# Performance work log

Measured on AMD Instinct MI355X. Metric: run time of the kernel, lower is better.

Reference implementation:

```python
import jax, jax.numpy as jnp
import numpy as np

B, N, C, H = 8, 2048, 512, 8
D = C // H                      # head dim = 64
Q_LENGTHS = [1024 + 128 * i for i in range(B)]  # ragged: 1024..1920, sum below
TQ = sum(Q_LENGTHS)             # 11776 total queries


def setup_inputs() -> dict:
    key = jax.random.key(0)
    ks = jax.random.split(key, 5)
    w = 0.02  # init scale for weights
    return {
        "x": jax.random.normal(ks[0], (B, N, C), jnp.float32),
        "q": jax.random.normal(ks[1], (TQ, C), jnp.float32),
        "Wq": jax.random.normal(ks[2], (C, C), jnp.float32) * w,
        "Wkv": jax.random.normal(ks[3], (2 * C, C), jnp.float32) * w,
        "Wproj": jax.random.normal(ks[4], (C, C), jnp.float32) * w,
        "bproj": jnp.zeros((C,), jnp.float32),
        "q_lengths": jnp.array(Q_LENGTHS, jnp.int32),
        "max_q_len": max(Q_LENGTHS),
    }


def reference(x, q, Wq, Wkv, Wproj, bproj, q_lengths, max_q_len):
    # Eval path of Attention.forward: batched_sparse_attention(q, k, v, q_lengths, scale)
    # == varlen cross-attention: queries of batch b attend over all N kv tokens of batch b.
    Tq = q.shape[0]
    scale = D ** -0.5

    qh = (q @ Wq.T).reshape(Tq, H, D)                 # [Tq, H, D]
    kv = (x @ Wkv.T).reshape(B, N, 2, H, D)
    k = kv[:, :, 0]                                   # [B, N, H, D]
    v = kv[:, :, 1]                                   # [B, N, H, D]

    # ragged -> padded per-batch layout
    csum = jnp.cumsum(q_lengths)                      # [B]
    offs = jnp.concatenate([jnp.zeros((1,), csum.dtype), csum])
    tok = jnp.arange(Tq)
    q_batch = (tok[:, None] >= csum[None, :]).sum(-1)  # [Tq] batch id per query
    q_pos = tok - offs[q_batch]                        # [Tq] position within batch

    qpad = jnp.zeros((B, max_q_len, H, D), qh.dtype).at[q_batch, q_pos].set(qh)

    scores = jnp.einsum('blhd,bnhd->bhln', qpad, k) * scale  # [B, H, L, N]
    attn = jax.nn.softmax(scores, axis=-1)                   # all N keys valid
    out = jnp.einsum('bhln,bnhd->blhd', attn, v)             # [B, L, H, D]

    out = out[q_batch, q_pos].reshape(Tq, C)           # gather ragged rows back
    return out @ Wproj.T + bproj
```

## Files before the change

### kernel.cpp

```cpp
#include <hip/hip_runtime.h>
#include <hip/hip_bf16.h>
#include <math.h>

constexpr int Cc = 512;
constexpr int Hh = 8;
constexpr int Dd = 64;
constexpr int Nn = 2048;
constexpr int Bb = 8;
constexpr int GK = 512;

typedef __attribute__((ext_vector_type(8))) short short8;
typedef __attribute__((ext_vector_type(4))) float f32x4;
typedef __attribute__((ext_vector_type(4))) unsigned int u32x4;
typedef __attribute__((ext_vector_type(2))) unsigned int u32x2;

#define C2SCALE 0.1803368801f

static __device__ __forceinline__ ushort f2bf(float v) {
  __hip_bfloat16 h = __float2bfloat16(v);
  return *reinterpret_cast<ushort*>(&h);
}
static __device__ __forceinline__ float bf2f(ushort u) {
  __hip_bfloat16 h = *reinterpret_cast<__hip_bfloat16*>(&u);
  return __bfloat162float(h);
}
static __device__ __forceinline__ unsigned int pk2(float f0, float f1) {
  return (unsigned int)f2bf(f0) | ((unsigned int)f2bf(f1) << 16);
}

template <int MODE, int TERMS, bool AF32, bool BF32>
__global__ __launch_bounds__(256) void mfma_nt2_kernel(
    const void* __restrict__ A0p, const void* __restrict__ A1p,
    const void* __restrict__ B0p, const void* __restrict__ B1p,
    const float* __restrict__ bias, float* __restrict__ Cf,
    ushort* __restrict__ Chi, int Nc)
{
  __shared__ ushort lAh[128 * 32];
  __shared__ ushort lBh[128 * 32];
  __shared__ ushort lAl[TERMS == 3 ? 128 * 32 : 1];
  __shared__ ushort lBl[TERMS == 3 ? 128 * 32 : 1];

  const int tid = threadIdx.x;
  const int w = tid >> 6, lane = tid & 63;
  const int c = lane & 15, g = lane >> 4;
  const int wr = (w >> 1) * 64, wc = (w & 1) * 64;
  const int m0 = blockIdx.y * 128, n0 = blockIdx.x * 128;
  const int sr = tid >> 2;
  const int sk = (tid & 3) * 8;

  short8 rAh[2], rAl[2], rBh[2], rBl[2];

  auto ldf32 = [&](const float* F, size_t idx, short8& h, short8& l) {
    const float4 f0 = *(const float4*)(F + idx);
    const float4 f1 = *(const float4*)(F + idx + 4);
    const float vv[8] = {f0.x, f0.y, f0.z, f0.w, f1.x, f1.y, f1.z, f1.w};
#pragma unroll
    for (int j = 0; j < 8; ++j) {
      const ushort hb = f2bf(vv[j]);
      ((ushort*)&h)[j] = hb;
      if (TERMS == 3) ((ushort*)&l)[j] = f2bf(vv[j] - bf2f(hb));
    }
  };

  auto loadA = [&](int k0) {
#pragma unroll
    for (int hf = 0; hf < 2; ++hf) {
      const size_t idx = (size_t)(m0 + sr + hf * 64) * GK + k0 + sk;
      if (AF32) {
        ldf32((const float*)A0p, idx, rAh[hf], rAl[hf]);
      } else {
        rAh[hf] = *(const short8*)((const ushort*)A0p + idx);
        if (TERMS == 3) rAl[hf] = *(const short8*)((const ushort*)A1p + idx);
      }
    }
  };
  auto loadB = [&](int k0) {
#pragma unroll
    for (int hf = 0; hf < 2; ++hf) {
      const size_t idx = (size_t)(n0 + sr + hf * 64) * GK + k0 + sk;
      if (BF32) {
        ldf32((const float*)B0p, idx, rBh[hf], rBl[hf]);
      } else {
        rBh[hf] = *(const short8*)((const ushort*)B0p + idx);
        if (TERMS == 3) rBl[hf] = *(const short8*)((const ushort*)B1p + idx);
      }
    }
  };

  f32x4 acc[4][4] = {};
  loadA(0);
  loadB(0);

  for (int k0 = 0; k0 < GK; k0 += 32) {
    __syncthreads();
    *(short8*)&lAh[sr * 32 + sk]        = rAh[0];
    *(short8*)&lAh[(sr + 64) * 32 + sk] = rAh[1];
    *(short8*)&lBh[sr * 32 + sk]        = rBh[0];
    *(short8*)&lBh[(sr + 64) * 32 + sk] = rBh[1];
    if (TERMS == 3) {
      *(short8*)&lAl[sr * 32 + sk]        = rAl[0];
      *(short8*)&lAl[(sr + 64) * 32 + sk] = rAl[1];
      *(short8*)&lBl[sr * 32 + sk]        = rBl[0];
      *(short8*)&lBl[(sr + 64) * 32 + sk] = rBl[1];
    }
    __syncthreads();
    if (k0 + 32 < GK) { loadA(k0 + 32); loadB(k0 + 32); }

    short8 ah[4], al[4], bh[4], bl[4];
#pragma unroll
    for (int i = 0; i < 4; ++i) {
      const int ar = (wr + i * 16 + c) * 32 + g * 8;
      const int br = (wc + i * 16 + c) * 32 + g * 8;
      ah[i] = *(const short8*)&lAh[ar];
      bh[i] = *(const short8*)&lBh[br];
      if (TERMS == 3) {
        al[i] = *(const short8*)&lAl[ar];
        bl[i] = *(const short8*)&lBl[br];
      }
    }
#pragma unroll
    for (int mi = 0; mi < 4; ++mi)
#pragma unroll
      for (int nj = 0; nj < 4; ++nj) {
        if (TERMS == 3) {
          acc[mi][nj] = __builtin_amdgcn_mfma_f32_16x16x32_bf16(ah[mi], bl[nj], acc[mi][nj], 0,0,0);
          acc[mi][nj] = __builtin_amdgcn_mfma_f32_16x16x32_bf16(al[mi], bh[nj], acc[mi][nj], 0,0,0);
        }
        acc[mi][nj] = __builtin_amdgcn_mfma_f32_16x16x32_bf16(ah[mi], bh[nj], acc[mi][nj], 0,0,0);
      }
  }

#pragma unroll
  for (int mi = 0; mi < 4; ++mi) {
#pragma unroll
    for (int r = 0; r < 4; ++r) {
      const size_t rb = (size_t)(m0 + wr + mi * 16 + g * 4 + r) * Nc;
#pragma unroll
      for (int nj = 0; nj < 4; ++nj) {
        const int col = n0 + wc + nj * 16 + c;
        const float v = acc[mi][nj][r];
        if (MODE == 0) {
          Cf[rb + col] = v + bias[col];
        } else if (MODE == 1) {
          Chi[rb + col] = f2bf(v);
        } else {
          Chi[rb + col] = f2bf(v * C2SCALE);
        }
      }
    }
  }
}

__global__ __launch_bounds__(512, 4) void attn_mfma11_kernel(
    const ushort* __restrict__ qhi,
    const ushort* __restrict__ kbf,
    const ushort* __restrict__ vtb,
    ushort* __restrict__ ohi,
    ushort* __restrict__ olo)
{
  constexpr int QOFF[8] = {0, 1024, 2176, 3456, 4864, 6400, 8064, 9856};

  const int lin = blockIdx.x;
  const int b  = lin & 7;
  const int h  = (lin >> 3) & 7;
  const int qt = lin >> 6;

  const int Lb  = 1024 + 128 * b;
  const int off = QOFF[b];
  if (qt * 128 >= Lb) return;

  constexpr int KP = 72;
  constexpr int VP = 136;
  constexpr int NC = Nn / 128;
  __shared__ ushort Ks[128 * KP];
  __shared__ ushort Vs[64 * VP];

  const int tid = threadIdx.x;
  const int lane = tid & 63;
  const int w = tid >> 6;
  const int c = lane & 15;
  const int g = (lane >> 4) & 3;

  short8 qf[2];
  const int qrow = off + qt * 128 + w * 16 + c;
  {
    const size_t base = (size_t)qrow * Cc + h * Dd + g * 8;
    qf[0] = *(const short8*)(qhi + base);
    qf[1] = *(const short8*)(qhi + base + 32);
  }

  float l_part = 0.f;
  f32x4 accO4[4] = {};

  const size_t kbase = (size_t)b * Nn * Cc + h * Dd;
  const size_t vbase = (size_t)h * Dd * (Bb * Nn) + (size_t)b * Nn;

  for (int ch = 0; ch < NC; ++ch) {
    __syncthreads();
#pragma unroll
    for (int it = 0; it < 2; ++it) {
      const int i = tid + it * 512;
      const int row = i >> 3, c8 = (i & 7) * 8;
      *(short8*)&Ks[row * KP + c8] =
          *(const short8*)&kbf[kbase + (size_t)(ch * 128 + row) * Cc + c8];
    }
#pragma unroll
    for (int it = 0; it < 2; ++it) {
      const int i = tid + it * 512;
      const int row = i >> 4, c8 = (i & 15) * 8;
      const int kb1 = (c8 & ~31) | (((c8 >> 3) & 3) << 2);
      const size_t gb = vbase + (size_t)row * (Bb * Nn) + ch * 128;
      const u32x2 vlo = *(const u32x2*)&vtb[gb + kb1];
      const u32x2 vhi = *(const u32x2*)&vtb[gb + kb1 + 16];
      u32x4 vv;
      vv[0] = vlo[0]; vv[1] = vlo[1];
      vv[2] = vhi[0]; vv[3] = vhi[1];
      *(short8*)&Vs[row * VP + c8] = __builtin_bit_cast(short8, vv);
    }
    __syncthreads();

#pragma unroll
    for (int st = 0; st < 2; ++st) {
      f32x4 accT4[4] = {};
      __builtin_amdgcn_s_setprio(1);
#pragma unroll
      for (int ks2 = 0; ks2 < 2; ++ks2) {
#pragma unroll
        for (int kb = 0; kb < 4; ++kb) {
          const short8 kf = *(const short8*)
              &Ks[(st * 64 + kb * 16 + c) * KP + ks2 * 32 + g * 8];
          accT4[kb] = __builtin_amdgcn_mfma_f32_16x16x32_bf16(kf, qf[ks2], accT4[kb], 0,0,0);
        }
      }
      __builtin_amdgcn_s_setprio(0);

      unsigned int up[4][2];
#pragma unroll
      for (int kb = 0; kb < 4; ++kb) {
        const float p0 = __builtin_amdgcn_exp2f(accT4[kb][0]);
        const float p1 = __builtin_amdgcn_exp2f(accT4[kb][1]);
        const float p2 = __builtin_amdgcn_exp2f(accT4[kb][2]);
        const float p3 = __builtin_amdgcn_exp2f(accT4[kb][3]);
        l_part += (p0 + p1) + (p2 + p3);
        up[kb][0] = pk2(p0, p1);
        up[kb][1] = pk2(p2, p3);
      }

#pragma unroll
      for (int ks2 = 0; ks2 < 2; ++ks2) {
        u32x4 wv;
        wv.x = up[2 * ks2][0];
        wv.y = up[2 * ks2][1];
        wv.z = up[2 * ks2 + 1][0];
        wv.w = up[2 * ks2 + 1][1];
        const short8 pa = __builtin_bit_cast(short8, wv);
        __builtin_amdgcn_s_setprio(1);
#pragma unroll
        for (int db = 0; db < 4; ++db) {
          const short8 vf = *(const short8*)
              &Vs[(db * 16 + c) * VP + st * 64 + ks2 * 32 + g * 8];
          accO4[db] = __builtin_amdgcn_mfma_f32_16x16x32_bf16(vf, pa, accO4[db], 0,0,0);
        }
        __builtin_amdgcn_s_setprio(0);
      }
    }
  }

  float l = l_part;
  l += __shfl_xor(l, 16);
  l += __shfl_xor(l, 32);
  const float inv = 1.f / l;
  const size_t rb = (size_t)qrow * Cc + h * Dd;
#pragma unroll
  for (int db = 0; db < 4; ++db) {
    const int d0 = db * 16 + g * 4;
    ushort4 uh, ul;
#pragma unroll
    for (int e = 0; e < 4; ++e) {
      const float o = accO4[db][e] * inv;
      const ushort hb = f2bf(o);
      ((ushort*)&uh)[e] = hb;
      ((ushort*)&ul)[e] = f2bf(o - bf2f(hb));
    }
    *(ushort4*)&ohi[rb + d0] = uh;
    *(ushort4*)&olo[rb + d0] = ul;
  }
}

extern "C" void kernel_launch(void* const* d_in, const int* in_sizes, int n_in,
                              void* d_out, int out_size, void* d_ws, size_t ws_size,
                              hipStream_t stream)
{
  const float* x     = (const float*)d_in[0];
  const float* q     = (const float*)d_in[1];
  const float* Wq    = (const float*)d_in[2];
  const float* Wkv   = (const float*)d_in[3];
  const float* Wproj = (const float*)d_in[4];
  const float* bproj = (const float*)d_in[5];

  const int TQ = in_sizes[1] / Cc;
  const int BN = in_sizes[0] / Cc;

  const float* Wv = Wkv + (size_t)Cc * Cc;

  const size_t szQ = (size_t)TQ * Cc * 2;
  const size_t szX = (size_t)BN * Cc * 2;

  char* p = (char*)d_ws;
  ushort* q_hi  = (ushort*)p;  p += szQ;
  ushort* k_bf  = (ushort*)p;  p += szX;
  ushort* v_t   = (ushort*)p;  p += szX;
  ushort* at_hi = (ushort*)p;  p += szQ;
  ushort* at_lo = (ushort*)p;

  mfma_nt2_kernel<2, 1, true, true><<<dim3(Cc/128, TQ/128), 256, 0, stream>>>(
      q, nullptr, Wq, nullptr, nullptr, nullptr, q_hi, Cc);
  mfma_nt2_kernel<1, 1, true, true><<<dim3(Cc/128, BN/128), 256, 0, stream>>>(
      x, nullptr, Wkv, nullptr, nullptr, nullptr, k_bf, Cc);
  mfma_nt2_kernel<1, 1, true, true><<<dim3(BN/128, Cc/128), 256, 0, stream>>>(
      Wv, nullptr, x, nullptr, nullptr, nullptr, v_t, BN);
  attn_mfma11_kernel<<<dim3(64 * 15), 512, 0, stream>>>(
      q_hi, k_bf, v_t, at_hi, at_lo);
  mfma_nt2_kernel<0, 3, false, true><<<dim3(Cc/128, TQ/128), 256, 0, stream>>>(
      at_hi, at_lo, Wproj, nullptr, bproj, (float*)d_out, nullptr, Cc);
}
```

Measured before the change: 191.5 us.

## Have each attention wave handle two 16-query tiles, halving block threads

The attention kernel now runs 256 threads per block instead of 512. Each wave processes 32 query rows as two 16-row tiles and reuses every K and V fragment read from LDS for two MFMAs. This halves LDS fragment reads per MFMA and the per-row share of synchronisation. In exchange it doubles the accumulator and probability registers per thread, which may hurt occupancy, and each thread issues twice as many global loads to fill the K/V tiles.

```diff
diff --git a/kernel.cpp b/kernel.cpp
--- a/kernel.cpp
+++ b/kernel.cpp
@@ -151,7 +151,7 @@
   }
 }
 
-__global__ __launch_bounds__(512, 4) void attn_mfma11_kernel(
+__global__ __launch_bounds__(256, 4) void attn_mfma12_kernel(
     const ushort* __restrict__ qhi,
     const ushort* __restrict__ kbf,
     const ushort* __restrict__ vtb,
@@ -181,16 +181,18 @@
   const int c = lane & 15;
   const int g = (lane >> 4) & 3;
 
-  short8 qf[2];
-  const int qrow = off + qt * 128 + w * 16 + c;
-  {
-    const size_t base = (size_t)qrow * Cc + h * Dd + g * 8;
-    qf[0] = *(const short8*)(qhi + base);
-    qf[1] = *(const short8*)(qhi + base + 32);
-  }
-
-  float l_part = 0.f;
-  f32x4 accO4[4] = {};
+  short8 qf[2][2];
+  int qrow[2];
+#pragma unroll
+  for (int t = 0; t < 2; ++t) {
+    qrow[t] = off + qt * 128 + w * 32 + t * 16 + c;
+    const size_t base = (size_t)qrow[t] * Cc + h * Dd + g * 8;
+    qf[t][0] = *(const short8*)(qhi + base);
+    qf[t][1] = *(const short8*)(qhi + base + 32);
+  }
+
+  float l_part[2] = {0.f, 0.f};
+  f32x4 accO4[2][4] = {};
 
   const size_t kbase = (size_t)b * Nn * Cc + h * Dd;
   const size_t vbase = (size_t)h * Dd * (Bb * Nn) + (size_t)b * Nn;
@@ -198,15 +200,15 @@
   for (int ch = 0; ch < NC; ++ch) {
     __syncthreads();
 #pragma unroll
-    for (int it = 0; it < 2; ++it) {
-      const int i = tid + it * 512;
+    for (int it = 0; it < 4; ++it) {
+      const int i = tid + it * 256;
       const int row = i >> 3, c8 = (i & 7) * 8;
       *(short8*)&Ks[row * KP + c8] =
           *(const short8*)&kbf[kbase + (size_t)(ch * 128 + row) * Cc + c8];
     }
 #pragma unroll
-    for (int it = 0; it < 2; ++it) {
-      const int i = tid + it * 512;
+    for (int it = 0; it < 4; ++it) {
+      const int i = tid + it * 256;
       const int row = i >> 4, c8 = (i & 15) * 8;
       const int kb1 = (c8 & ~31) | (((c8 >> 3) & 3) << 2);
       const size_t gb = vbase + (size_t)row * (Bb * Nn) + ch * 128;
@@ -221,7 +223,7 @@
 
 #pragma unroll
     for (int st = 0; st < 2; ++st) {
-      f32x4 accT4[4] = {};
+      f32x4 accT4[2][4] = {};
       __builtin_amdgcn_s_setprio(1);
 #pragma unroll
       for (int ks2 = 0; ks2 < 2; ++ks2) {
@@ -229,61 +231,72 @@
         for (int kb = 0; kb < 4; ++kb) {
           const short8 kf = *(const short8*)
               &Ks[(st * 64 + kb * 16 + c) * KP + ks2 * 32 + g * 8];
-          accT4[kb] = __builtin_amdgcn_mfma_f32_16x16x32_bf16(kf, qf[ks2], accT4[kb], 0,0,0);
+          accT4[0][kb] = __builtin_amdgcn_mfma_f32_16x16x32_bf16(kf, qf[0][ks2], accT4[0][kb], 0,0,0);
+          accT4[1][kb] = __builtin_amdgcn_mfma_f32_16x16x32_bf16(kf, qf[1][ks2], accT4[1][kb], 0,0,0);
         }
       }
       __builtin_amdgcn_s_setprio(0);
 
-      unsigned int up[4][2];
-#pragma unroll
-      for (int kb = 0; kb < 4; ++kb) {
-        const float p0 = __builtin_amdgcn_exp2f(accT4[kb][0]);
-        const float p1 = __builtin_amdgcn_exp2f(accT4[kb][1]);
-        const float p2 = __builtin_amdgcn_exp2f(accT4[kb][2]);
-        const float p3 = __builtin_amdgcn_exp2f(accT4[kb][3]);
-        l_part += (p0 + p1) + (p2 + p3);
-        up[kb][0] = pk2(p0, p1);
-        up[kb][1] = pk2(p2, p3);
-      }
+      unsigned int up[2][4][2];
+#pragma unroll
+      for (int t = 0; t < 2; ++t)
+#pragma unroll
+        for (int kb = 0; kb < 4; ++kb) {
+          const float p0 = __builtin_amdgcn_exp2f(accT4[t][kb][0]);
+          const float p1 = __builtin_amdgcn_exp2f(accT4[t][kb][1]);
+          const float p2 = __builtin_amdgcn_exp2f(accT4[t][kb][2]);
+          const float p3 = __builtin_amdgcn_exp2f(accT4[t][kb][3]);
+          l_part[t] += (p0 + p1) + (p2 + p3);
+          up[t][kb][0] = pk2(p0, p1);
+          up[t][kb][1] = pk2(p2, p3);
+        }
 
 #pragma unroll
       for (int ks2 = 0; ks2 < 2; ++ks2) {
-        u32x4 wv;
-        wv.x = up[2 * ks2][0];
-        wv.y = up[2 * ks2][1];
-        wv.z = up[2 * ks2 + 1][0];
-        wv.w = up[2 * ks2 + 1][1];
-        const short8 pa = __builtin_bit_cast(short8, wv);
+        short8 pa[2];
+#pragma unroll
+        for (int t = 0; t < 2; ++t) {
+          u32x4 wv;
+          wv.x = up[t][2 * ks2][0];
+          wv.y = up[t][2 * ks2][1];
+          wv.z = up[t][2 * ks2 + 1][0];
+          wv.w = up[t][2 * ks2 + 1][1];
+          pa[t] = __builtin_bit_cast(short8, wv);
+        }
         __builtin_amdgcn_s_setprio(1);
 #pragma unroll
         for (int db = 0; db < 4; ++db) {
           const short8 vf = *(const short8*)
               &Vs[(db * 16 + c) * VP + st * 64 + ks2 * 32 + g * 8];
-          accO4[db] = __builtin_amdgcn_mfma_f32_16x16x32_bf16(vf, pa, accO4[db], 0,0,0);
+          accO4[0][db] = __builtin_amdgcn_mfma_f32_16x16x32_bf16(vf, pa[0], accO4[0][db], 0,0,0);
+          accO4[1][db] = __builtin_amdgcn_mfma_f32_16x16x32_bf16(vf, pa[1], accO4[1][db], 0,0,0);
         }
         __builtin_amdgcn_s_setprio(0);
       }
     }
   }
 
-  float l = l_part;
-  l += __shfl_xor(l, 16);
-  l += __shfl_xor(l, 32);
-  const float inv = 1.f / l;
-  const size_t rb = (size_t)qrow * Cc + h * Dd;
-#pragma unroll
-  for (int db = 0; db < 4; ++db) {
-    const int d0 = db * 16 + g * 4;
-    ushort4 uh, ul;
-#pragma unroll
-    for (int e = 0; e < 4; ++e) {
-      const float o = accO4[db][e] * inv;
-      const ushort hb = f2bf(o);
-      ((ushort*)&uh)[e] = hb;
-      ((ushort*)&ul)[e] = f2bf(o - bf2f(hb));
-    }
-    *(ushort4*)&ohi[rb + d0] = uh;
-    *(ushort4*)&olo[rb + d0] = ul;
+#pragma unroll
+  for (int t = 0; t < 2; ++t) {
+    float l = l_part[t];
+    l += __shfl_xor(l, 16);
+    l += __shfl_xor(l, 32);
+    const float inv = 1.f / l;
+    const size_t rb = (size_t)qrow[t] * Cc + h * Dd;
+#pragma unroll
+    for (int db = 0; db < 4; ++db) {
+      const int d0 = db * 16 + g * 4;
+      ushort4 uh, ul;
+#pragma unroll
+      for (int e = 0; e < 4; ++e) {
+        const float o = accO4[t][db][e] * inv;
+        const ushort hb = f2bf(o);
+        ((ushort*)&uh)[e] = hb;
+        ((ushort*)&ul)[e] = f2bf(o - bf2f(hb));
+      }
+      *(ushort4*)&ohi[rb + d0] = uh;
+      *(ushort4*)&olo[rb + d0] = ul;
+    }
   }
 }
 
@@ -319,7 +332,7 @@
       x, nullptr, Wkv, nullptr, nullptr, nullptr, k_bf, Cc);
   mfma_nt2_kernel<1, 1, true, true><<<dim3(BN/128, Cc/128), 256, 0, stream>>>(
       Wv, nullptr, x, nullptr, nullptr, nullptr, v_t, BN);
-  attn_mfma11_kernel<<<dim3(64 * 15), 512, 0, stream>>>(
+  attn_mfma12_kernel<<<dim3(64 * 15), 256, 0, stream>>>(
       q_hi, k_bf, v_t, at_hi, at_lo);
   mfma_nt2_kernel<0, 3, false, true><<<dim3(Cc/128, TQ/128), 256, 0, stream>>>(
       at_hi, at_lo, Wproj, nullptr, bproj, (float*)d_out, nullptr, Cc);
```

Result: faster. 186.4 us (-2.7%).
